# Optimization experiments

Hardware: AMD Instinct MI355X
Metric: run time of the kernel (lower is better)

The kernel has to match this reference:

```python
import jax, jax.numpy as jnp
import numpy as np
from jax import lax

S, B, I, H, L, O, T = 128, 64, 1024, 1024, 2, 1024, 64


def lstm_cell(x, h, c, wih, whh, b):
    # PyTorch gate order: i, f, g, o
    g = x @ wih.T + h @ whh.T + b  # [B, 4H]
    i, f, gg, o = jnp.split(g, 4, axis=-1)
    c = jax.nn.sigmoid(f) * c + jax.nn.sigmoid(i) * jnp.tanh(gg)
    h = jax.nn.sigmoid(o) * jnp.tanh(c)
    return h, c


def run_lstm_seq(xs, wih, whh, b):
    # xs: [S, B, in]; zero initial state (torch default)
    h0 = jnp.zeros((xs.shape[1], whh.shape[-1]), xs.dtype)

    def step(carry, x):
        h, c = lstm_cell(x, carry[0], carry[1], wih, whh, b)
        return (h, c), h

    (h, c), ys = lax.scan(step, (h0, h0), xs)
    return ys, h, c


def setup_inputs() -> dict:
    key = jax.random.key(0)
    ks = jax.random.split(key, 10)
    s = 1.0 / np.sqrt(H)
    u = lambda k, shape: jax.random.uniform(k, shape, minval=-s, maxval=s, dtype=jnp.float32)
    return {
        "input_seq": jax.random.normal(ks[0], (S, B, I), dtype=jnp.float32),
        "enc_wih": u(ks[1], (L, 4 * H, I)),
        "enc_whh": u(ks[2], (L, 4 * H, H)),
        "enc_b": u(ks[3], (L, 4 * H)),
        "dec_wih": u(ks[4], (L, 4 * H, I)),
        "dec_whh": u(ks[5], (L, 4 * H, H)),
        "dec_b": u(ks[6], (L, 4 * H)),
        "lin_w": u(ks[7], (O, H)),
        "lin_b": u(ks[8], (O,)),
        "target_seq_length": T,
    }


def reference(input_seq, enc_wih, enc_whh, enc_b, dec_wih, dec_whh, dec_b, lin_w, lin_b, target_seq_length):
    # ---- encoder: stacked LSTM over the full sequence ----
    xs = input_seq
    hs, cs = [], []
    for l in range(L):
        xs, h, c = run_lstm_seq(xs, enc_wih[l], enc_whh[l], enc_b[l])
        hs.append(h)
        cs.append(c)
    hs = jnp.stack(hs)  # [L, B, H]
    cs = jnp.stack(cs)

    x0 = input_seq[-1]  # [B, I]

    def dec_step(carry, _):
        x, hs, cs = carry
        inp = x
        nh, nc = [], []
        for l in range(L):
            h, c = lstm_cell(inp, hs[l], cs[l], dec_wih[l], dec_whh[l], dec_b[l])
            nh.append(h)
            nc.append(c)
            inp = h
        y = inp @ lin_w.T + lin_b  # [B, O]
        return (y, jnp.stack(nh), jnp.stack(nc)), y

    _, outs = lax.scan(dec_step, (x0, hs, cs), None, length=target_seq_length)
    return jnp.transpose(outs, (1, 0, 2))  # [B, T, O]
```

## Files before the change

### kernel.cpp

```cpp
#include <hip/hip_runtime.h>
#include <math.h>


typedef unsigned short u16;
typedef short short8 __attribute__((ext_vector_type(8)));
typedef float f32x4 __attribute__((ext_vector_type(4)));

#define MFMA_BF16 __builtin_amdgcn_mfma_f32_16x16x32_bf16

__device__ __forceinline__ u16 f2bf(float x) {
  unsigned u = __builtin_bit_cast(unsigned, x);
  unsigned r = u + 0x7fffu + ((u >> 16) & 1u);
  return (u16)(r >> 16);
}
__device__ __forceinline__ float bf2f(u16 b) {
  return __builtin_bit_cast(float, ((unsigned)b) << 16);
}
__device__ __forceinline__ int permrow(int r) {
  int gate = r >> 10, hc = r & 1023;
  return ((hc >> 2) << 4) + ((hc & 3) << 2) + gate;
}


__global__ void split_mat(const float* __restrict__ src, u16* __restrict__ dh,
                          u16* __restrict__ dl, int n, int mode) {
  int i = blockIdx.x * 256 + threadIdx.x;
  if (i >= n) return;
  float v = src[i];
  u16 hi = f2bf(v);
  u16 lo = f2bf(v - bf2f(hi));
  int r = i >> 10, c = i & 1023;
  int idx = i;
  if (mode == 1) idx = c * 1024 + r;
  else if (mode == 2) idx = permrow(r) * 1024 + c;
  dh[idx] = hi; dl[idx] = lo;
}

__global__ void zero_f4(float4* __restrict__ p, int n) {
  int i = blockIdx.x * 256 + threadIdx.x;
  if (i < n) p[i] = make_float4(0.f, 0.f, 0.f, 0.f);
}

__global__ void bias_perm(const float* __restrict__ in, float* __restrict__ out) {
  int i = blockIdx.x * 256 + threadIdx.x;
  if (i < 4096) out[permrow(i)] = in[i];
}

__global__ void bias_comb(const float* __restrict__ db0, const float* __restrict__ lb,
                          const float* __restrict__ wih, float* __restrict__ out) {
  __shared__ float red[256];
  int n = blockIdx.x;
  float s = 0.f;
  for (int k = threadIdx.x; k < 1024; k += 256) s += lb[k] * wih[(size_t)n * 1024 + k];
  red[threadIdx.x] = s;
  __syncthreads();
  for (int d = 128; d > 0; d >>= 1) {
    if (threadIdx.x < d) red[threadIdx.x] += red[threadIdx.x + d];
    __syncthreads();
  }
  if (threadIdx.x == 0) out[permrow(n)] = db0[n] + red[0];
}

template<int MT>
__global__ __launch_bounds__(256) void gemm_split(
    const u16* __restrict__ Ah, const u16* __restrict__ Al, int lda,
    const u16* __restrict__ Bh, const u16* __restrict__ Bl, int ldb,
    int K, int gn,
    u16* __restrict__ Ch, u16* __restrict__ Cl, int ldc,
    float* __restrict__ outp, const float* __restrict__ bias, int ldout, int mode) {
  int bm = blockIdx.x / gn, bn = blockIdx.x % gn;
  int l = threadIdx.x & 63, w = threadIdx.x >> 6;
  int n0 = bn * 128 + w * 32;
  int rr = l & 15, ko = (l >> 4) << 3, q = l >> 4;
  int M0 = bm * 64 * MT;
  f32x4 acc[8 * MT] = {};
  for (int kk = 0; kk < K; kk += 32) {
    short8 bh[2], bl[2];
#pragma unroll
    for (int nt = 0; nt < 2; ++nt) {
      size_t bo = (size_t)(n0 + nt * 16 + rr) * ldb + kk + ko;
      bh[nt] = *(const short8*)(Bh + bo);
      bl[nt] = *(const short8*)(Bl + bo);
    }
#pragma unroll
    for (int mt = 0; mt < 4 * MT; ++mt) {
      size_t ao = (size_t)(M0 + mt * 16 + rr) * lda + kk + ko;
      short8 ah = *(const short8*)(Ah + ao);
      short8 al = *(const short8*)(Al + ao);
#pragma unroll
      for (int nt = 0; nt < 2; ++nt) {
        f32x4 t = acc[mt * 2 + nt];
        t = MFMA_BF16(ah, bh[nt], t, 0, 0, 0);
        t = MFMA_BF16(ah, bl[nt], t, 0, 0, 0);
        t = MFMA_BF16(al, bh[nt], t, 0, 0, 0);
        acc[mt * 2 + nt] = t;
      }
    }
  }
#pragma unroll
  for (int mt = 0; mt < 4 * MT; ++mt)
#pragma unroll
    for (int nt = 0; nt < 2; ++nt)
#pragma unroll
      for (int r = 0; r < 4; ++r) {
        int row = M0 + mt * 16 + q * 4 + r;
        int col = n0 + nt * 16 + rr;
        float v = acc[mt * 2 + nt][r];
        if (mode == 0) {
          u16 hh = f2bf(v);
          Ch[(size_t)row * ldc + col] = hh;
          Cl[(size_t)row * ldc + col] = f2bf(v - bf2f(hh));
        } else if (mode == 1) {
          int t = row >> 6, b = row & 63;
          outp[(size_t)b * 65536 + t * 1024 + col] = v + bias[col];
        } else {
          outp[(size_t)row * ldout + col] = v;
        }
      }
}


struct Half {
  const u16 *Ah, *Al, *Wh, *Wl;
  const float* pre;
  const float* bias;
  float* c;
  u16 *Hh, *Hl;
  int active;
};

__global__ __launch_bounds__(512, 1) void lstm_pair(Half hA, Half hB) {
  int j = blockIdx.x;
  Half S = (j < 128) ? hA : hB;
  if (!S.active) return;
  int sub = j & 127;
  int rowblk = ((sub & 7) << 4) | (sub >> 3);
  int R = rowblk << 5;
  int tid = threadIdx.x;
  int l = tid & 63, w = tid >> 6;
  int rr = l & 15, ko = (l >> 4) << 3, q = l >> 4;
  int kb = w << 7;
  const u16* __restrict__ Wh = S.Wh + (size_t)(R + rr) * 1024 + kb + ko;
  const u16* __restrict__ Wl = S.Wl + (size_t)(R + rr) * 1024 + kb + ko;
  const u16* __restrict__ Ah = S.Ah + kb + ko;
  const u16* __restrict__ Al = S.Al + kb + ko;

  f32x4 acc[8] = {};
#pragma unroll
  for (int kk = 0; kk < 128; kk += 32) {
    short8 bh[2], bl[2];
#pragma unroll
    for (int nt = 0; nt < 2; ++nt) {
      bh[nt] = *(const short8*)(Wh + (size_t)(nt << 4) * 1024 + kk);
      bl[nt] = *(const short8*)(Wl + (size_t)(nt << 4) * 1024 + kk);
    }
#pragma unroll
    for (int mt = 0; mt < 4; ++mt) {
      size_t ao = (size_t)((mt << 4) + rr) * 1024 + kk;
      short8 ah = *(const short8*)(Ah + ao);
      short8 al = *(const short8*)(Al + ao);
#pragma unroll
      for (int nt = 0; nt < 2; ++nt) {
        f32x4 t = acc[mt * 2 + nt];
        t = MFMA_BF16(ah, bh[nt], t, 0, 0, 0);
        t = MFMA_BF16(ah, bl[nt], t, 0, 0, 0);
        t = MFMA_BF16(al, bh[nt], t, 0, 0, 0);
        acc[mt * 2 + nt] = t;
      }
    }
  }

  __shared__ float lds[8][64][33];
#pragma unroll
  for (int mt = 0; mt < 4; ++mt)
#pragma unroll
    for (int nt = 0; nt < 2; ++nt)
#pragma unroll
      for (int r = 0; r < 4; ++r)
        lds[w][(mt << 4) + (q << 2) + r][(nt << 4) + rr] = acc[mt * 2 + nt][r];
  __syncthreads();

  int b = tid >> 3, e = tid & 7;
  float g[4];
#pragma unroll
  for (int gt = 0; gt < 4; ++gt) {
    int c = (e << 2) + gt;
    float s = S.bias[R + c] + S.pre[(size_t)b * 4096 + R + c];
#pragma unroll
    for (int ww = 0; ww < 8; ++ww) s += lds[ww][b][c];
    g[gt] = s;
  }
  int hc = (rowblk << 3) + e;
  size_t ci = (size_t)b * 1024 + hc;
  float cold = S.c[ci];
  float is = 1.f / (1.f + expf(-g[0]));
  float fs = 1.f / (1.f + expf(-g[1]));
  float gg = tanhf(g[2]);
  float os = 1.f / (1.f + expf(-g[3]));
  float cn = fs * cold + is * gg;
  S.c[ci] = cn;
  float h = os * tanhf(cn);
  S.Hh[ci] = f2bf(h);
  S.Hl[ci] = f2bf(h - bf2f(f2bf(h)));
}


struct Op { const u16 *Ah, *Al, *Wh, *Wl; };
struct Stage1 {
  Op ops[2];
  int nops;
  const float* pre;
  const float* bias;
  float* c;
  u16 *Hh, *Hl, *Gh, *Gl;
};

__global__ __launch_bounds__(512, 1) void lstm_one(Stage1 S) {
  int j = blockIdx.x;
  int rowblk = ((j & 7) << 5) | (j >> 3);
  int R = rowblk << 4;
  int tid = threadIdx.x;
  int l = tid & 63, w = tid >> 6;
  int rr = l & 15, ko = (l >> 4) << 3, q = l >> 4;
  int kslices = 8 / S.nops;
  int kwidth = 1024 / kslices;
  Op op = S.ops[w / kslices];
  int kb = (w % kslices) * kwidth;
  const u16* __restrict__ Wh = op.Wh + (size_t)(R + rr) * 1024 + kb + ko;
  const u16* __restrict__ Wl = op.Wl + (size_t)(R + rr) * 1024 + kb + ko;
  const u16* __restrict__ Ah = op.Ah + kb + ko;
  const u16* __restrict__ Al = op.Al + kb + ko;

  f32x4 acc[4] = {};
#pragma unroll 2
  for (int kk = 0; kk < kwidth; kk += 32) {
    short8 bh = *(const short8*)(Wh + kk);
    short8 bl = *(const short8*)(Wl + kk);
#pragma unroll
    for (int mt = 0; mt < 4; ++mt) {
      size_t ao = (size_t)((mt << 4) + rr) * 1024 + kk;
      short8 ah = *(const short8*)(Ah + ao);
      short8 al = *(const short8*)(Al + ao);
      acc[mt] = MFMA_BF16(ah, bh, acc[mt], 0, 0, 0);
      acc[mt] = MFMA_BF16(ah, bl, acc[mt], 0, 0, 0);
      acc[mt] = MFMA_BF16(al, bh, acc[mt], 0, 0, 0);
    }
  }

  __shared__ float lds[8][64][17];
#pragma unroll
  for (int mt = 0; mt < 4; ++mt)
#pragma unroll
    for (int r = 0; r < 4; ++r)
      lds[w][(mt << 4) + (q << 2) + r][rr] = acc[mt][r];
  __syncthreads();

  if (tid < 256) {
    int b = tid >> 2, e = tid & 3;
    float g[4];
#pragma unroll
    for (int gt = 0; gt < 4; ++gt) {
      int c = (e << 2) + gt;
      float s = S.bias[R + c];
      if (S.pre) s += S.pre[(size_t)b * 4096 + R + c];
#pragma unroll
      for (int ww = 0; ww < 8; ++ww) s += lds[ww][b][c];
      g[gt] = s;
    }
    int hc = (rowblk << 2) + e;
    size_t ci = (size_t)b * 1024 + hc;
    float cold = S.c[ci];
    float is = 1.f / (1.f + expf(-g[0]));
    float fs = 1.f / (1.f + expf(-g[1]));
    float gg = tanhf(g[2]);
    float os = 1.f / (1.f + expf(-g[3]));
    float cn = fs * cold + is * gg;
    S.c[ci] = cn;
    float h = os * tanhf(cn);
    u16 hh = f2bf(h);
    u16 hl = f2bf(h - bf2f(hh));
    S.Hh[ci] = hh; S.Hl[ci] = hl;
    if (S.Gh) { S.Gh[ci] = hh; S.Gl[ci] = hl; }
  }
}


extern "C" void kernel_launch(void* const* d_in, const int* in_sizes, int n_in,
                              void* d_out, int out_size, void* d_ws, size_t ws_size,
                              hipStream_t stream) {
  (void)in_sizes; (void)n_in; (void)out_size; (void)ws_size;
  const float* input_seq = (const float*)d_in[0];
  const float* enc_wih   = (const float*)d_in[1];
  const float* enc_whh   = (const float*)d_in[2];
  const float* enc_b     = (const float*)d_in[3];
  const float* dec_wih   = (const float*)d_in[4];
  const float* dec_whh   = (const float*)d_in[5];
  const float* dec_b     = (const float*)d_in[6];
  const float* lin_w     = (const float*)d_in[7];
  const float* lin_b     = (const float*)d_in[8];
  float* out = (float*)d_out;

  const size_t WE = 4096ull * 1024;
  const size_t HB = 64ull * 1024;
  char* ws = (char*)d_ws;
  size_t off = 0;
  auto alloc16 = [&](size_t elems) {
    u16* p = (u16*)(ws + off);
    off = (off + elems * 2 + 255) & ~(size_t)255;
    return p;
  };
  auto allocf = [&](size_t elems) {
    float* p = (float*)(ws + off);
    off = (off + elems * 4 + 255) & ~(size_t)255;
    return p;
  };

  u16 *WihE0h = alloc16(WE), *WihE0l = alloc16(WE);
  u16 *WhhE0h = alloc16(WE), *WhhE0l = alloc16(WE);
  u16 *WihE1h = alloc16(WE), *WihE1l = alloc16(WE);
  u16 *WhhE1h = alloc16(WE), *WhhE1l = alloc16(WE);
  u16 *WihD0h = alloc16(WE), *WihD0l = alloc16(WE);
  u16 *WhhD0h = alloc16(WE), *WhhD0l = alloc16(WE);
  u16 *WihD1h = alloc16(WE), *WihD1l = alloc16(WE);
  u16 *WhhD1h = alloc16(WE), *WhhD1l = alloc16(WE);
  u16 *Wcombh = alloc16(WE), *Wcombl = alloc16(WE);
  u16 *WLh  = alloc16(1024 * 1024), *WLl  = alloc16(1024 * 1024);
  u16 *WLTh = alloc16(1024 * 1024), *WLTl = alloc16(1024 * 1024);
  u16 *XCh = alloc16(16 * HB), *XCl = alloc16(16 * HB);
  u16 *XLh = alloc16(HB), *XLl = alloc16(HB);
  u16 *H0ch = alloc16(17 * HB), *H0cl = alloc16(17 * HB);
  u16 *H1h = alloc16(64 * HB), *H1l = alloc16(64 * HB);
  size_t zbeg = off;
  u16 *zh = alloc16(HB), *zl = alloc16(HB);
  float *c0 = allocf(HB), *c1 = allocf(HB);
  size_t zend = off;
  u16 *e1h = alloc16(2 * HB), *e1l = alloc16(2 * HB);
  u16 *d0h = alloc16(2 * HB), *d0l = alloc16(2 * HB);
  u16 *d1h = alloc16(2 * HB), *d1l = alloc16(2 * HB);
  float *G0 = allocf(1024ull * 4096);
  float *G1 = allocf(1024ull * 4096);
  float *Gd0 = allocf(64 * 4096);
  float *ebp0 = allocf(4096), *ebp1 = allocf(4096);
  float *dbp0 = allocf(4096), *dbp1 = allocf(4096);
  float *bdec0 = allocf(4096);

  {
    int n4 = (int)((zend - zbeg) / 16);
    zero_f4<<<dim3((n4 + 255) / 256), dim3(256), 0, stream>>>((float4*)(ws + zbeg), n4);
  }
  auto split = [&](const float* src, u16* dh, u16* dl, int n, int mode) {
    split_mat<<<dim3((n + 255) / 256), dim3(256), 0, stream>>>(src, dh, dl, n, mode);
  };
  split(enc_wih,        WihE0h, WihE0l, (int)WE, 2);
  split(enc_whh,        WhhE0h, WhhE0l, (int)WE, 2);
  split(enc_wih + WE,   WihE1h, WihE1l, (int)WE, 2);
  split(enc_whh + WE,   WhhE1h, WhhE1l, (int)WE, 2);
  split(dec_wih,        WihD0h, WihD0l, (int)WE, 2);
  split(dec_whh,        WhhD0h, WhhD0l, (int)WE, 2);
  split(dec_wih + WE,   WihD1h, WihD1l, (int)WE, 2);
  split(dec_whh + WE,   WhhD1h, WhhD1l, (int)WE, 2);
  split(lin_w, WLh,  WLl,  1024 * 1024, 0);
  split(lin_w, WLTh, WLTl, 1024 * 1024, 1);
  split(input_seq + 127ull * HB, XLh, XLl, (int)HB, 0);
  bias_perm<<<dim3(16), dim3(256), 0, stream>>>(enc_b,        ebp0);
  bias_perm<<<dim3(16), dim3(256), 0, stream>>>(enc_b + 4096, ebp1);
  bias_perm<<<dim3(16), dim3(256), 0, stream>>>(dec_b,        dbp0);
  bias_perm<<<dim3(16), dim3(256), 0, stream>>>(dec_b + 4096, dbp1);
  bias_comb<<<dim3(4096), dim3(256), 0, stream>>>(dec_b, lin_b, dec_wih, bdec0);
  gemm_split<2><<<dim3(32 * 8), dim3(256), 0, stream>>>(
      WihD0h, WihD0l, 1024, WLTh, WLTl, 1024, 1024, 8,
      Wcombh, Wcombl, 1024, nullptr, nullptr, 0, 0);
  gemm_split<1><<<dim3(32), dim3(256), 0, stream>>>(
      XLh, XLl, 1024, WihD0h, WihD0l, 1024, 1024, 32,
      nullptr, nullptr, 0, Gd0, nullptr, 4096, 2);

  for (int ch = 0; ch < 8; ++ch) {
    split(input_seq + (size_t)ch * 16 * HB, XCh, XCl, (int)(16 * HB), 0);
    gemm_split<2><<<dim3(8 * 32), dim3(256), 0, stream>>>(
        XCh, XCl, 1024, WihE0h, WihE0l, 1024, 1024, 32,
        nullptr, nullptr, 0, G0, nullptr, 4096, 2);
    for (int lt = 0; lt < 16; ++lt) {
      int t0 = ch * 16 + lt;
      int t1 = (ch - 1) * 16 + lt;
      Half A;
      A.Ah = (t0 == 0) ? zh : (lt == 0 ? H0ch + 16ull * HB : H0ch + (size_t)lt * HB);
      A.Al = (t0 == 0) ? zl : (lt == 0 ? H0cl + 16ull * HB : H0cl + (size_t)lt * HB);
      A.Wh = WhhE0h; A.Wl = WhhE0l;
      A.pre = G0 + (size_t)lt * 64 * 4096;
      A.bias = ebp0; A.c = c0;
      A.Hh = H0ch + (size_t)(lt + 1) * HB; A.Hl = H0cl + (size_t)(lt + 1) * HB;
      A.active = 1;
      Half B;
      B.Ah = (t1 == 0) ? zh : e1h + (size_t)((t1 - 1) & 1) * HB;
      B.Al = (t1 == 0) ? zl : e1l + (size_t)((t1 - 1) & 1) * HB;
      B.Wh = WhhE1h; B.Wl = WhhE1l;
      B.pre = G1 + (size_t)lt * 64 * 4096;
      B.bias = ebp1; B.c = c1;
      B.Hh = e1h + (size_t)((t1 >= 0 ? t1 : 0) & 1) * HB;
      B.Hl = e1l + (size_t)((t1 >= 0 ? t1 : 0) & 1) * HB;
      B.active = (ch >= 1) ? 1 : 0;
      lstm_pair<<<dim3(256), dim3(512), 0, stream>>>(A, B);
    }
    gemm_split<2><<<dim3(8 * 32), dim3(256), 0, stream>>>(
        H0ch + HB, H0cl + HB, 1024, WihE1h, WihE1l, 1024, 1024, 32,
        nullptr, nullptr, 0, G1, nullptr, 4096, 2);
  }
  for (int lt = 0; lt < 16; ++lt) {
    int t1 = 112 + lt;
    Half A; A.active = 0;
    A.Ah = zh; A.Al = zl; A.Wh = WhhE0h; A.Wl = WhhE0l;
    A.pre = G0; A.bias = ebp0; A.c = c0; A.Hh = H0ch; A.Hl = H0cl;
    Half B;
    B.Ah = e1h + (size_t)((t1 - 1) & 1) * HB;
    B.Al = e1l + (size_t)((t1 - 1) & 1) * HB;
    B.Wh = WhhE1h; B.Wl = WhhE1l;
    B.pre = G1 + (size_t)lt * 64 * 4096;
    B.bias = ebp1; B.c = c1;
    B.Hh = e1h + (size_t)(t1 & 1) * HB;
    B.Hl = e1l + (size_t)(t1 & 1) * HB;
    B.active = 1;
    lstm_pair<<<dim3(256), dim3(512), 0, stream>>>(A, B);
  }

  for (int t = 0; t < 64; ++t) {
    const u16 *h0p_h = (t == 0) ? H0ch + 16ull * HB : d0h + (size_t)((t - 1) & 1) * HB;
    const u16 *h0p_l = (t == 0) ? H0cl + 16ull * HB : d0l + (size_t)((t - 1) & 1) * HB;
    const u16 *h1p_h = (t == 0) ? e1h + HB : d1h + (size_t)((t - 1) & 1) * HB;
    const u16 *h1p_l = (t == 0) ? e1l + HB : d1l + (size_t)((t - 1) & 1) * HB;
    Stage1 A;
    if (t == 0) {
      A.ops[0] = {h0p_h, h0p_l, WhhD0h, WhhD0l};
      A.ops[1] = A.ops[0];
      A.nops = 1; A.pre = Gd0; A.bias = dbp0;
    } else {
      A.ops[0] = {h1p_h, h1p_l, Wcombh, Wcombl};
      A.ops[1] = {h0p_h, h0p_l, WhhD0h, WhhD0l};
      A.nops = 2; A.pre = nullptr; A.bias = bdec0;
    }
    A.c = c0;
    A.Hh = d0h + (size_t)(t & 1) * HB; A.Hl = d0l + (size_t)(t & 1) * HB;
    A.Gh = nullptr; A.Gl = nullptr;
    lstm_one<<<dim3(256), dim3(512), 0, stream>>>(A);
    Stage1 Bst;
    Bst.ops[0] = {d0h + (size_t)(t & 1) * HB, d0l + (size_t)(t & 1) * HB, WihD1h, WihD1l};
    Bst.ops[1] = {h1p_h, h1p_l, WhhD1h, WhhD1l};
    Bst.nops = 2; Bst.pre = nullptr; Bst.bias = dbp1; Bst.c = c1;
    Bst.Hh = d1h + (size_t)(t & 1) * HB; Bst.Hl = d1l + (size_t)(t & 1) * HB;
    Bst.Gh = H1h + (size_t)t * HB; Bst.Gl = H1l + (size_t)t * HB;
    lstm_one<<<dim3(256), dim3(512), 0, stream>>>(Bst);
  }

  gemm_split<2><<<dim3(32 * 8), dim3(256), 0, stream>>>(
      H1h, H1l, 1024, WLh, WLl, 1024, 1024, 8,
      nullptr, nullptr, 0, out, lin_b, 1024, 1);
}
```

Measured before the change: 6.569 ms.

## Fuse decoder timesteps into one persistent kernel with grid barriers and register-resident weights

Replaces the 128 per-step decoder launches with a single persistent kernel of 256 blocks that loops over all 64 timesteps and synchronises both layers through atomic grid barriers. Each wave keeps its slice of the decoder weights (hi/lo bf16 halves) in registers across all steps, so weights are not re-read from memory every step. At t=0 the combined-weight operand reads a zero hidden state so one code path serves every step. This removes kernel launch overhead and weight reloads, but needs all 256 blocks co-resident for the spin barrier, adds register pressure, and each barrier's atomic spin costs some latency.

```diff
diff --git a/kernel.cpp b/kernel.cpp
--- a/kernel.cpp
+++ b/kernel.cpp
@@ -205,82 +205,176 @@
 }
 
 
-struct Op { const u16 *Ah, *Al, *Wh, *Wl; };
-struct Stage1 {
-  Op ops[2];
-  int nops;
-  const float* pre;
-  const float* bias;
-  float* c;
-  u16 *Hh, *Hl, *Gh, *Gl;
+struct DecP {
+  const u16 *Wch, *Wcl;
+  const u16 *W0h, *W0l;
+  const u16 *Wi1h, *Wi1l;
+  const u16 *Wh1h, *Wh1l;
+  const u16 *h0i_h, *h0i_l;
+  const u16 *h1i_h, *h1i_l;
+  const u16 *zh, *zl;
+  const float *Gd0, *dbp0, *bdec0, *dbp1;
+  float *c0, *c1;
+  u16 *d0h, *d0l, *d1h, *d1l;
+  u16 *H1h, *H1l;
+  int* bar;
 };
 
-__global__ __launch_bounds__(512, 1) void lstm_one(Stage1 S) {
+__device__ __forceinline__ void gridbar(int* b, int nb) {
+  __syncthreads();
+  if (threadIdx.x == 0) {
+    __hip_atomic_fetch_add(b, 1, __ATOMIC_RELEASE, __HIP_MEMORY_SCOPE_AGENT);
+    while (__hip_atomic_load(b, __ATOMIC_RELAXED, __HIP_MEMORY_SCOPE_AGENT) < nb)
+      __builtin_amdgcn_s_sleep(1);
+    __builtin_amdgcn_fence(__ATOMIC_ACQUIRE, "agent");
+  }
+  __syncthreads();
+}
+
+__global__ __launch_bounds__(512, 1) void lstm_dec_persist(DecP D) {
   int j = blockIdx.x;
   int rowblk = ((j & 7) << 5) | (j >> 3);
   int R = rowblk << 4;
   int tid = threadIdx.x;
   int l = tid & 63, w = tid >> 6;
   int rr = l & 15, ko = (l >> 4) << 3, q = l >> 4;
-  int kslices = 8 / S.nops;
-  int kwidth = 1024 / kslices;
-  Op op = S.ops[w / kslices];
-  int kb = (w % kslices) * kwidth;
-  const u16* __restrict__ Wh = op.Wh + (size_t)(R + rr) * 1024 + kb + ko;
-  const u16* __restrict__ Wl = op.Wl + (size_t)(R + rr) * 1024 + kb + ko;
-  const u16* __restrict__ Ah = op.Ah + kb + ko;
-  const u16* __restrict__ Al = op.Al + kb + ko;
-
-  f32x4 acc[4] = {};
-#pragma unroll 2
-  for (int kk = 0; kk < kwidth; kk += 32) {
-    short8 bh = *(const short8*)(Wh + kk);
-    short8 bl = *(const short8*)(Wl + kk);
-#pragma unroll
-    for (int mt = 0; mt < 4; ++mt) {
-      size_t ao = (size_t)((mt << 4) + rr) * 1024 + kk;
-      short8 ah = *(const short8*)(Ah + ao);
-      short8 al = *(const short8*)(Al + ao);
-      acc[mt] = MFMA_BF16(ah, bh, acc[mt], 0, 0, 0);
-      acc[mt] = MFMA_BF16(ah, bl, acc[mt], 0, 0, 0);
-      acc[mt] = MFMA_BF16(al, bh, acc[mt], 0, 0, 0);
-    }
+  int opidx = w >> 2;
+  int kb = (w & 3) << 8;
+  size_t woff = (size_t)(R + rr) * 1024 + kb + ko;
+
+  const u16* pWAh = (opidx == 0 ? D.Wch : D.W0h) + woff;
+  const u16* pWAl = (opidx == 0 ? D.Wcl : D.W0l) + woff;
+  const u16* pWBh = (opidx == 0 ? D.Wi1h : D.Wh1h) + woff;
+  const u16* pWBl = (opidx == 0 ? D.Wi1l : D.Wh1l) + woff;
+  short8 wAh[8], wAl[8], wBh[8], wBl[8];
+#pragma unroll
+  for (int ki = 0; ki < 8; ++ki) {
+    wAh[ki] = *(const short8*)(pWAh + (ki << 5));
+    wAl[ki] = *(const short8*)(pWAl + (ki << 5));
+    wBh[ki] = *(const short8*)(pWBh + (ki << 5));
+    wBl[ki] = *(const short8*)(pWBl + (ki << 5));
   }
 
   __shared__ float lds[8][64][17];
-#pragma unroll
-  for (int mt = 0; mt < 4; ++mt)
-#pragma unroll
-    for (int r = 0; r < 4; ++r)
-      lds[w][(mt << 4) + (q << 2) + r][rr] = acc[mt][r];
-  __syncthreads();
-
-  if (tid < 256) {
-    int b = tid >> 2, e = tid & 3;
-    float g[4];
-#pragma unroll
-    for (int gt = 0; gt < 4; ++gt) {
-      int c = (e << 2) + gt;
-      float s = S.bias[R + c];
-      if (S.pre) s += S.pre[(size_t)b * 4096 + R + c];
-#pragma unroll
-      for (int ww = 0; ww < 8; ++ww) s += lds[ww][b][c];
-      g[gt] = s;
-    }
-    int hc = (rowblk << 2) + e;
-    size_t ci = (size_t)b * 1024 + hc;
-    float cold = S.c[ci];
-    float is = 1.f / (1.f + expf(-g[0]));
-    float fs = 1.f / (1.f + expf(-g[1]));
-    float gg = tanhf(g[2]);
-    float os = 1.f / (1.f + expf(-g[3]));
-    float cn = fs * cold + is * gg;
-    S.c[ci] = cn;
-    float h = os * tanhf(cn);
-    u16 hh = f2bf(h);
-    u16 hl = f2bf(h - bf2f(hh));
-    S.Hh[ci] = hh; S.Hl[ci] = hl;
-    if (S.Gh) { S.Gh[ci] = hh; S.Gl[ci] = hl; }
+  const u16 *h0p_h = D.h0i_h, *h0p_l = D.h0i_l;
+  const u16 *h1p_h = D.h1i_h, *h1p_l = D.h1i_l;
+
+  for (int t = 0; t < 64; ++t) {
+    u16* d0c_h = D.d0h + (size_t)(t & 1) * 65536;
+    u16* d0c_l = D.d0l + (size_t)(t & 1) * 65536;
+    u16* d1c_h = D.d1h + (size_t)(t & 1) * 65536;
+    u16* d1c_l = D.d1l + (size_t)(t & 1) * 65536;
+
+    {
+      const u16* Aph = (opidx == 0) ? (t == 0 ? D.zh : h1p_h) : h0p_h;
+      const u16* Apl = (opidx == 0) ? (t == 0 ? D.zl : h1p_l) : h0p_l;
+      const u16* __restrict__ Ah_ = Aph + kb + ko;
+      const u16* __restrict__ Al_ = Apl + kb + ko;
+      f32x4 acc[4] = {};
+#pragma unroll
+      for (int ki = 0; ki < 8; ++ki) {
+#pragma unroll
+        for (int mt = 0; mt < 4; ++mt) {
+          size_t ao = (size_t)((mt << 4) + rr) * 1024 + (ki << 5);
+          short8 ah = *(const short8*)(Ah_ + ao);
+          short8 al = *(const short8*)(Al_ + ao);
+          acc[mt] = MFMA_BF16(ah, wAh[ki], acc[mt], 0, 0, 0);
+          acc[mt] = MFMA_BF16(ah, wAl[ki], acc[mt], 0, 0, 0);
+          acc[mt] = MFMA_BF16(al, wAh[ki], acc[mt], 0, 0, 0);
+        }
+      }
+#pragma unroll
+      for (int mt = 0; mt < 4; ++mt)
+#pragma unroll
+        for (int r = 0; r < 4; ++r)
+          lds[w][(mt << 4) + (q << 2) + r][rr] = acc[mt][r];
+    }
+    __syncthreads();
+    if (tid < 256) {
+      int b = tid >> 2, e = tid & 3;
+      float g[4];
+#pragma unroll
+      for (int gt = 0; gt < 4; ++gt) {
+        int c = (e << 2) + gt;
+        float s = (t == 0)
+            ? D.dbp0[R + c] + D.Gd0[(size_t)b * 4096 + R + c]
+            : D.bdec0[R + c];
+#pragma unroll
+        for (int ww = 0; ww < 8; ++ww) s += lds[ww][b][c];
+        g[gt] = s;
+      }
+      int hc = (rowblk << 2) + e;
+      size_t ci = (size_t)b * 1024 + hc;
+      float cold = D.c0[ci];
+      float is = 1.f / (1.f + expf(-g[0]));
+      float fs = 1.f / (1.f + expf(-g[1]));
+      float gg = tanhf(g[2]);
+      float os = 1.f / (1.f + expf(-g[3]));
+      float cn = fs * cold + is * gg;
+      D.c0[ci] = cn;
+      float h = os * tanhf(cn);
+      u16 hh = f2bf(h);
+      d0c_h[ci] = hh;
+      d0c_l[ci] = f2bf(h - bf2f(hh));
+    }
+    gridbar(D.bar + 2 * t, 256);
+
+    {
+      const u16* Aph = (opidx == 0) ? d0c_h : h1p_h;
+      const u16* Apl = (opidx == 0) ? d0c_l : h1p_l;
+      const u16* __restrict__ Ah_ = Aph + kb + ko;
+      const u16* __restrict__ Al_ = Apl + kb + ko;
+      f32x4 acc[4] = {};
+#pragma unroll
+      for (int ki = 0; ki < 8; ++ki) {
+#pragma unroll
+        for (int mt = 0; mt < 4; ++mt) {
+          size_t ao = (size_t)((mt << 4) + rr) * 1024 + (ki << 5);
+          short8 ah = *(const short8*)(Ah_ + ao);
+          short8 al = *(const short8*)(Al_ + ao);
+          acc[mt] = MFMA_BF16(ah, wBh[ki], acc[mt], 0, 0, 0);
+          acc[mt] = MFMA_BF16(ah, wBl[ki], acc[mt], 0, 0, 0);
+          acc[mt] = MFMA_BF16(al, wBh[ki], acc[mt], 0, 0, 0);
+        }
+      }
+#pragma unroll
+      for (int mt = 0; mt < 4; ++mt)
+#pragma unroll
+        for (int r = 0; r < 4; ++r)
+          lds[w][(mt << 4) + (q << 2) + r][rr] = acc[mt][r];
+    }
+    __syncthreads();
+    if (tid < 256) {
+      int b = tid >> 2, e = tid & 3;
+      float g[4];
+#pragma unroll
+      for (int gt = 0; gt < 4; ++gt) {
+        int c = (e << 2) + gt;
+        float s = D.dbp1[R + c];
+#pragma unroll
+        for (int ww = 0; ww < 8; ++ww) s += lds[ww][b][c];
+        g[gt] = s;
+      }
+      int hc = (rowblk << 2) + e;
+      size_t ci = (size_t)b * 1024 + hc;
+      float cold = D.c1[ci];
+      float is = 1.f / (1.f + expf(-g[0]));
+      float fs = 1.f / (1.f + expf(-g[1]));
+      float gg = tanhf(g[2]);
+      float os = 1.f / (1.f + expf(-g[3]));
+      float cn = fs * cold + is * gg;
+      D.c1[ci] = cn;
+      float h = os * tanhf(cn);
+      u16 hh = f2bf(h);
+      u16 hl = f2bf(h - bf2f(hh));
+      d1c_h[ci] = hh; d1c_l[ci] = hl;
+      size_t hidx = (size_t)t * 65536 + ci;
+      D.H1h[hidx] = hh; D.H1l[hidx] = hl;
+    }
+    if (t != 63) gridbar(D.bar + 2 * t + 1, 256);
+
+    h0p_h = d0c_h; h0p_l = d0c_l;
+    h1p_h = d1c_h; h1p_l = d1c_l;
   }
 }
 
@@ -333,6 +427,8 @@
   size_t zbeg = off;
   u16 *zh = alloc16(HB), *zl = alloc16(HB);
   float *c0 = allocf(HB), *c1 = allocf(HB);
+  int *barbuf = (int*)(ws + off);
+  off = (off + 128 * sizeof(int) + 255) & ~(size_t)255;
   size_t zend = off;
   u16 *e1h = alloc16(2 * HB), *e1l = alloc16(2 * HB);
   u16 *d0h = alloc16(2 * HB), *d0l = alloc16(2 * HB);
@@ -422,32 +518,21 @@
     lstm_pair<<<dim3(256), dim3(512), 0, stream>>>(A, B);
   }
 
-  for (int t = 0; t < 64; ++t) {
-    const u16 *h0p_h = (t == 0) ? H0ch + 16ull * HB : d0h + (size_t)((t - 1) & 1) * HB;
-    const u16 *h0p_l = (t == 0) ? H0cl + 16ull * HB : d0l + (size_t)((t - 1) & 1) * HB;
-    const u16 *h1p_h = (t == 0) ? e1h + HB : d1h + (size_t)((t - 1) & 1) * HB;
-    const u16 *h1p_l = (t == 0) ? e1l + HB : d1l + (size_t)((t - 1) & 1) * HB;
-    Stage1 A;
-    if (t == 0) {
-      A.ops[0] = {h0p_h, h0p_l, WhhD0h, WhhD0l};
-      A.ops[1] = A.ops[0];
-      A.nops = 1; A.pre = Gd0; A.bias = dbp0;
-    } else {
-      A.ops[0] = {h1p_h, h1p_l, Wcombh, Wcombl};
-      A.ops[1] = {h0p_h, h0p_l, WhhD0h, WhhD0l};
-      A.nops = 2; A.pre = nullptr; A.bias = bdec0;
-    }
-    A.c = c0;
-    A.Hh = d0h + (size_t)(t & 1) * HB; A.Hl = d0l + (size_t)(t & 1) * HB;
-    A.Gh = nullptr; A.Gl = nullptr;
-    lstm_one<<<dim3(256), dim3(512), 0, stream>>>(A);
-    Stage1 Bst;
-    Bst.ops[0] = {d0h + (size_t)(t & 1) * HB, d0l + (size_t)(t & 1) * HB, WihD1h, WihD1l};
-    Bst.ops[1] = {h1p_h, h1p_l, WhhD1h, WhhD1l};
-    Bst.nops = 2; Bst.pre = nullptr; Bst.bias = dbp1; Bst.c = c1;
-    Bst.Hh = d1h + (size_t)(t & 1) * HB; Bst.Hl = d1l + (size_t)(t & 1) * HB;
-    Bst.Gh = H1h + (size_t)t * HB; Bst.Gl = H1l + (size_t)t * HB;
-    lstm_one<<<dim3(256), dim3(512), 0, stream>>>(Bst);
+  {
+    DecP P;
+    P.Wch = Wcombh; P.Wcl = Wcombl;
+    P.W0h = WhhD0h; P.W0l = WhhD0l;
+    P.Wi1h = WihD1h; P.Wi1l = WihD1l;
+    P.Wh1h = WhhD1h; P.Wh1l = WhhD1l;
+    P.h0i_h = H0ch + 16ull * HB; P.h0i_l = H0cl + 16ull * HB;
+    P.h1i_h = e1h + HB; P.h1i_l = e1l + HB;
+    P.zh = zh; P.zl = zl;
+    P.Gd0 = Gd0; P.dbp0 = dbp0; P.bdec0 = bdec0; P.dbp1 = dbp1;
+    P.c0 = c0; P.c1 = c1;
+    P.d0h = d0h; P.d0l = d0l; P.d1h = d1h; P.d1l = d1l;
+    P.H1h = H1h; P.H1l = H1l;
+    P.bar = barbuf;
+    lstm_dec_persist<<<dim3(256), dim3(512), 0, stream>>>(P);
   }
 
   gemm_split<2><<<dim3(32 * 8), dim3(256), 0, stream>>>(
```

After: 7.822 ms. +19.1%, slower.
